# Performance work log

Measured on AMD Instinct MI355X. Metric: run time of the kernel, lower is better.

Reference implementation:

```python
import jax, jax.numpy as jnp
import numpy as np

B, S = 2, 2048          # packed prefill: 2 sequences of 2048 tokens
T = B * S
HID = 3584
H, KV, D = 16, 8, 256   # query heads, kv heads, head_dim (num_groups = 2)
SCALE = 256.0 ** -0.5   # query_pre_attn_scalar ** -0.5
SOFTCAP = 50.0
WINDOW = 1024           # sliding_window (window_size_left)
ROPE_THETA = 10000.0


def _rope_cos_sin():
    # TGI PositionRotaryEmbedding: per-token cos/sin of shape [T, D//2]
    inv_freq = 1.0 / (ROPE_THETA ** (np.arange(0, D, 2, dtype=np.float32) / D))
    pos = np.tile(np.arange(S, dtype=np.float32), B)  # positions restart per sequence
    freqs = pos[:, None] * inv_freq[None, :]          # [T, D/2]
    return jnp.asarray(np.cos(freqs)), jnp.asarray(np.sin(freqs))


def _apply_rope(x, cos, sin):
    # neox-style rotate-half; x: [T, h, D], cos/sin: [T, D/2]
    x1, x2 = x[..., : D // 2], x[..., D // 2 :]
    c, s = cos[:, None, :], sin[:, None, :]
    return jnp.concatenate([x1 * c - x2 * s, x2 * c + x1 * s], axis=-1)


def setup_inputs() -> dict:
    key = jax.random.key(0)
    k1, k2, k3 = jax.random.split(key, 3)
    cos, sin = _rope_cos_sin()
    return {
        "hidden_states": jax.random.normal(k1, (T, HID), dtype=jnp.float32),
        "cos": cos,
        "sin": sin,
        "w_qkv": jax.random.normal(k2, ((H + 2 * KV) * D, HID), dtype=jnp.float32) * 0.02,
        "w_o": jax.random.normal(k3, (HID, H * D), dtype=jnp.float32) * 0.02,
    }


def reference(hidden_states, cos, sin, w_qkv, w_o):
    qkv = hidden_states @ w_qkv.T                      # [T, (H+2KV)*D]
    q = qkv[:, : H * D].reshape(T, H, D)
    k = qkv[:, H * D : (H + KV) * D].reshape(T, KV, D)
    v = qkv[:, (H + KV) * D :].reshape(T, KV, D)

    q = _apply_rope(q, cos, sin)
    k = _apply_rope(k, cos, sin)

    # unpack varlen batch (equal-length sequences)
    q = q.reshape(B, S, H, D)
    # GQA: repeat each kv head num_groups=2 times (kv_head_mapping)
    k = jnp.repeat(k.reshape(B, S, KV, D), H // KV, axis=2)
    v = jnp.repeat(v.reshape(B, S, KV, D), H // KV, axis=2)

    scores = jnp.einsum("bqhd,bkhd->bhqk", q, k) * SCALE
    scores = SOFTCAP * jnp.tanh(scores / SOFTCAP)      # logit softcapping

    i = jnp.arange(S)[:, None]
    j = jnp.arange(S)[None, :]
    allowed = (j <= i) & (j >= i - WINDOW)             # causal + sliding window left
    scores = jnp.where(allowed[None, None], scores, jnp.finfo(scores.dtype).min)

    probs = jax.nn.softmax(scores, axis=-1)
    out = jnp.einsum("bhqk,bkhd->bqhd", probs, v)      # [B, S, H, D]
    return out.reshape(T, H * D) @ w_o.T               # [T, HID]
```

## Files before the change

kernel.cpp:

```cpp
#include <hip/hip_runtime.h>

typedef __bf16 bf16x8 __attribute__((ext_vector_type(8)));
typedef __bf16 bf16x4 __attribute__((ext_vector_type(4)));
typedef float  f32x4  __attribute__((ext_vector_type(4)));

#define AS1 __attribute__((address_space(1)))
#define AS3 __attribute__((address_space(3)))

__device__ __forceinline__ void async16(const void* g, void* l) {
  __builtin_amdgcn_global_load_lds((const AS1 void*)g, (AS3 void*)l, 16, 0, 0);
}

static constexpr int T_   = 4096;
static constexpr int Sq   = 2048;
static constexpr int HID  = 3584;
static constexpr int NH   = 16;
static constexpr int NKV  = 8;
static constexpr int DH   = 256;
static constexpr float SCALE_   = 0.0625f;
static constexpr float SOFTCAP_ = 50.0f;
static constexpr int WINDOW_    = 1024;

__global__ __launch_bounds__(256) void cast2_f32_bf16(const float4* __restrict__ a,
                                                      bf16x4* __restrict__ oa, int n4a,
                                                      const float4* __restrict__ b,
                                                      bf16x4* __restrict__ ob, int n4b) {
  int i = blockIdx.x * 256 + threadIdx.x;
  int stride = gridDim.x * 256;
  int ntot = n4a + n4b;
  for (; i < ntot; i += stride) {
    const float4 v = (i < n4a) ? a[i] : b[i - n4a];
    bf16x4 o;
    o[0] = (__bf16)v.x; o[1] = (__bf16)v.y; o[2] = (__bf16)v.z; o[3] = (__bf16)v.w;
    if (i < n4a) oa[i] = o; else ob[i - n4a] = o;
  }
}


#define VMW(N) do { asm volatile("s_waitcnt vmcnt(" #N ")" ::: "memory"); \
                    __builtin_amdgcn_sched_barrier(0); } while (0)

#define PHASE(SEL, CK, I0, KK, LOADB, STAGE)                                   \
  {                                                                            \
    bf16x8 a_[4];                                                              \
    _Pragma("unroll") for (int ii_ = 0; ii_ < 4; ++ii_)                        \
      a_[ii_] = *(const bf16x8*)&lA[SEL][aBase + (CK) + ((I0) + ii_) * 1024];  \
    if (LOADB) {                                                               \
      _Pragma("unroll") for (int j_ = 0; j_ < 4; ++j_)                         \
        bfr[j_][KK] = *(const bf16x8*)&lB[SEL][bBase + (CK) + j_ * 1024];      \
    }                                                                          \
    STAGE;                                                                     \
    __builtin_amdgcn_s_barrier();                                              \
    asm volatile("s_waitcnt lgkmcnt(0)" ::: "memory");                         \
    __builtin_amdgcn_sched_barrier(0);                                         \
    __builtin_amdgcn_s_setprio(1);                                             \
    _Pragma("unroll") for (int ii_ = 0; ii_ < 4; ++ii_)                        \
      _Pragma("unroll") for (int j_ = 0; j_ < 4; ++j_)                         \
        acc[(I0) + ii_][j_] = __builtin_amdgcn_mfma_f32_16x16x32_bf16(         \
            a_[ii_], bfr[j_][KK], acc[(I0) + ii_][j_], 0, 0, 0);               \
    __builtin_amdgcn_s_setprio(0);                                             \
    __builtin_amdgcn_sched_barrier(0);                                         \
    __builtin_amdgcn_s_barrier();                                              \
  }

template <bool OUT_BF16>
__global__ __launch_bounds__(512, 2) void gemm_bt8(const __bf16* __restrict__ A,
                                                   const __bf16* __restrict__ B,
                                                   __bf16* __restrict__ Cb,
                                                   float* __restrict__ Cf,
                                                   int M, int N, int K) {
  __shared__ __attribute__((aligned(16))) __bf16 lA[2][256 * 64];
  __shared__ __attribute__((aligned(16))) __bf16 lB[2][256 * 64];

  const int tid  = threadIdx.x;
  const int w    = tid >> 6;
  const int lane = tid & 63;
  const int wm   = w >> 2;
  const int wn   = w & 3;
  const int mrow = lane & 15;
  const int quad = lane >> 4;
  const int sw   = mrow & 7;

  const int gx = gridDim.x, gy = gridDim.y;
  const int orig = blockIdx.y * gx + blockIdx.x;
  int tileN, tileM;
  {
    int ccols, crows;
    if ((gx % 4) == 0 && (gy % 2) == 0)      { ccols = 4; crows = 2; }
    else if ((gx % 2) == 0 && (gy % 4) == 0) { ccols = 2; crows = 4; }
    else                                     { ccols = 1; crows = 1; }
    if (ccols * crows == 8) {
      const int cw = gx / ccols, ch = gy / crows;
      const int xcd = orig & 7, loc = orig >> 3;
      const int cx = xcd % ccols, cy = xcd / ccols;
      const int ln = loc % cw,    lm = loc / cw;
      tileN = (cx * cw + ln) * 256;
      tileM = (cy * ch + lm) * 256;
    } else {
      tileN = blockIdx.x * 256;
      tileM = blockIdx.y * 256;
    }
  }

  const int srow   = tid >> 3;
  const int schunk = (tid & 7) ^ (srow & 7);
  const int k64  = K << 6;
  const int k128 = K << 7;
  const __bf16* pa = A + (size_t)(tileM + srow) * K + schunk * 8;
  const __bf16* pb = B + (size_t)(tileN + srow) * K + schunk * 8;

  auto stage_half = [&](__bf16* lbase, int lrow, const __bf16* lanePtr, int koff) {
    async16(lanePtr + koff,       &lbase[(lrow + w * 8) * 64]);
    async16(lanePtr + koff + k64, &lbase[(lrow + 64 + w * 8) * 64]);
  };

  const int cK0 = (quad ^ sw) * 8;
  const int cK1 = cK0 ^ 32;
  const int aBase = (wm * 128 + mrow) * 64;
  const int bBase = (wn * 64 + mrow) * 64;

  f32x4 acc[8][4];
#pragma unroll
  for (int i = 0; i < 8; ++i)
#pragma unroll
    for (int j = 0; j < 4; ++j) acc[i][j] = (f32x4){0.f, 0.f, 0.f, 0.f};

  const int NT = K >> 6;
  const int NI = NT >> 1;

  stage_half(lB[0], 0,   pb, 0);
  stage_half(lB[0], 128, pb, k128);
  stage_half(lA[0], 0,   pa, 0);
  stage_half(lA[0], 128, pa, k128);
  stage_half(lB[1], 0,   pb, 64);
  stage_half(lB[1], 128, pb, 64 + k128);
  VMW(4);
  __builtin_amdgcn_s_barrier();

  for (int it = 0; it < NI; ++it) {
    const int t    = 2 * it;
    const bool more = (it + 1 < NI);
    const int kA1 = (t + 1) << 6;
    const int k2  = (t + 2) << 6;
    const int k3  = (t + 3) << 6;

    bf16x8 bfr[4][2];

    PHASE(0, cK0, 0, 0, true,
          { stage_half(lA[1], 0, pa, kA1); });
    PHASE(0, cK1, 0, 1, true,
          { stage_half(lA[1], 128, pa, kA1 + k128); });
    PHASE(0, cK0, 4, 0, false,
          { if (more) stage_half(lB[0], 0, pb, k2); });
    PHASE(0, cK1, 4, 1, false,
          { if (more) { stage_half(lB[0], 128, pb, k2 + k128); VMW(4); }
            else VMW(0); });
    PHASE(1, cK0, 0, 0, true,
          { if (more) stage_half(lA[0], 0, pa, k2); });
    PHASE(1, cK1, 0, 1, true,
          { if (more) stage_half(lA[0], 128, pa, k2 + k128); });
    PHASE(1, cK0, 4, 0, false,
          { if (more) stage_half(lB[1], 0, pb, k3); });
    PHASE(1, cK1, 4, 1, false,
          { if (more) { stage_half(lB[1], 128, pb, k3 + k128); VMW(4); }
            else VMW(0); });
  }

#pragma unroll
  for (int i = 0; i < 8; ++i) {
    const int row0 = tileM + wm * 128 + i * 16 + quad * 4;
#pragma unroll
    for (int j = 0; j < 4; ++j) {
      const int col = tileN + wn * 64 + j * 16 + mrow;
#pragma unroll
      for (int r = 0; r < 4; ++r) {
        if constexpr (OUT_BF16)
          Cb[(size_t)(row0 + r) * N + col] = (__bf16)acc[i][j][r];
        else
          Cf[(size_t)(row0 + r) * N + col] = acc[i][j][r];
      }
    }
  }
}

__global__ __launch_bounds__(256) void aux_fused(const __bf16* __restrict__ qkv,
                                                 const float* __restrict__ cosb,
                                                 const float* __restrict__ sinb,
                                                 __bf16* __restrict__ qout,
                                                 __bf16* __restrict__ kout,
                                                 __bf16* __restrict__ vt,
                                                 const float4* __restrict__ wo,
                                                 bf16x4* __restrict__ wo_bf) {
  __shared__ __bf16 tile[64][72];
  const int blk = blockIdx.x;
  const int tid = threadIdx.x;

  if (blk < 4096) {
    const int t = blk;
    const int b = t >> 11, s = t & (Sq - 1);
    const int d = tid & 127;
    const int half = tid >> 7;
    const float c  = cosb[t * 128 + d];
    const float sn = sinb[t * 128 + d];
    const size_t base = (size_t)t * 8192;
#pragma unroll
    for (int it = 0; it < 12; ++it) {
      int seg = it * 2 + half;
      float x1 = (float)qkv[base + seg * 256 + d];
      float x2 = (float)qkv[base + seg * 256 + 128 + d];
      float o1 = x1 * c - x2 * sn;
      float o2 = x2 * c + x1 * sn;
      if (seg < 16) {
        size_t o = ((size_t)(b * NH + seg) * Sq + s) * DH + d;
        qout[o] = (__bf16)o1;
        qout[o + 128] = (__bf16)o2;
      } else {
        int kvh = seg - 16;
        size_t o = ((size_t)(b * NKV + kvh) * Sq + s) * DH + d;
        kout[o] = (__bf16)o1;
        kout[o + 128] = (__bf16)o2;
      }
    }
  } else if (blk < 6144) {
    const int flat = blk - 4096;
    const int bx  = flat & 127;
    const int bkv = flat >> 7;
    const int b = bkv >> 3, kv = bkv & 7;
    const int st0 = (bx >> 2) * 64;
    const int dt0 = (bx & 3) * 64;
#pragma unroll
    for (int it = 0; it < 2; ++it) {
      int g = it * 256 + tid;
      int r = g >> 3, cc = (g & 7) * 8;
      const __bf16* src = qkv + (size_t)(b * Sq + st0 + r) * 8192 + 6144 + kv * 256 + dt0 + cc;
      bf16x8 v = *(const bf16x8*)src;
#pragma unroll
      for (int j = 0; j < 8; ++j) tile[r][cc + j] = v[j];
    }
    __syncthreads();
#pragma unroll
    for (int it = 0; it < 2; ++it) {
      int g = it * 256 + tid;
      int r = g >> 3, cc = (g & 7) * 8;
      bf16x8 v;
#pragma unroll
      for (int j = 0; j < 8; ++j) v[j] = tile[cc + j][r];
      *(bf16x8*)(vt + ((size_t)bkv * DH + dt0 + r) * Sq + st0 + cc) = v;
    }
  } else {
    const int n4 = HID * 4096 / 4;
    int i = (blk - 6144) * 256 + tid;
    const int stride = 1024 * 256;
    for (; i < n4; i += stride) {
      float4 v = wo[i];
      bf16x4 o;
      o[0] = (__bf16)v.x; o[1] = (__bf16)v.y; o[2] = (__bf16)v.z; o[3] = (__bf16)v.w;
      wo_bf[i] = o;
    }
  }
}

template <int MODE>
__device__ __forceinline__ void softcap_tile(const f32x4 sc[4], float lrun[4],
                                             __bf16* Pl, int pbase, int mrow,
                                             int kt, int qi) {
#pragma unroll
  for (int j = 0; j < 4; ++j) {
    const int kj = kt + j * 16 + mrow;
#pragma unroll
    for (int r = 0; r < 4; ++r) {
      float z = sc[j][r] * (SCALE_ / SOFTCAP_);
      float z2 = z * z;
      float u = __builtin_fmaf(z2, 0.13333333f, -0.33333333f);
      float th = z * __builtin_fmaf(z2, u, 1.0f);
      float pe = __builtin_fmaf(th, 72.134752f, -72.134752f);
      if (MODE == 1) pe = (kj <= qi + r) ? pe : -1000.0f;
      if (MODE == 2) pe = (kj >= qi + r - WINDOW_) ? pe : -1000.0f;
      float p = __builtin_amdgcn_exp2f(pe);
      lrun[r] += p;
      Pl[pbase + r * 72 + j * 16 + mrow] = (__bf16)p;
    }
  }
}

__global__ __launch_bounds__(256, 2) void attn_kernel(const __bf16* __restrict__ q,
                                                      const __bf16* __restrict__ k,
                                                      const __bf16* __restrict__ vt,
                                                      __bf16* __restrict__ out) {
  __shared__ __bf16 Kl[64 * 256];
  __shared__ __bf16 Vl[256 * 64];
  __shared__ __bf16 Pl[4 * 1152];

  const int bid0 = blockIdx.x;
  const int gidx = (bid0 & 7) * 128 + (bid0 >> 3);
  const int grp  = gidx >> 5;
  const int qt   = 31 - (gidx & 31);
  const int h    = grp & 15;
  const int b    = grp >> 4;
  const int kvh  = h >> 1;
  const int q0   = qt * 64;
  const int tid = threadIdx.x, w = tid >> 6, lane = tid & 63;
  const int mrow = lane & 15, quad = lane >> 4;
  const int sw = mrow & 7;

  bf16x8 qf[8];
  const __bf16* qbase = q + ((size_t)(b * NH + h) * Sq + q0 + w * 16 + mrow) * DH;
#pragma unroll
  for (int kf = 0; kf < 8; ++kf) qf[kf] = *(const bf16x8*)(qbase + kf * 32 + quad * 8);

  f32x4 o[16];
#pragma unroll
  for (int n = 0; n < 16; ++n) o[n] = (f32x4){0.f, 0.f, 0.f, 0.f};
  float lrun[4] = {0.f, 0.f, 0.f, 0.f};

  int kt_lo = q0 - WINDOW_; if (kt_lo < 0) kt_lo = 0;
  const __bf16* kbase = k + (size_t)(b * NKV + kvh) * Sq * DH;
  const __bf16* vbase = vt + (size_t)(b * NKV + kvh) * DH * Sq;
  const int qi = q0 + w * 16 + quad * 4;
  const int pbase = w * 1152 + quad * 4 * 72;

  for (int kt = kt_lo; kt <= q0; kt += 64) {
#pragma unroll
    for (int it = 0; it < 8; ++it) {
      int g = it * 256 + tid;
      int rk = g >> 5, uk = g & 31;
      const __bf16* gk = kbase + (size_t)(kt + rk) * DH + (uk ^ (rk & 7)) * 8;
      async16(gk, &Kl[(it * 256 + w * 64) * 8]);
    }
#pragma unroll
    for (int it = 0; it < 8; ++it) {
      int g = it * 256 + tid;
      int rv = g >> 3, uv = g & 7;
      const __bf16* gv = vbase + (size_t)rv * Sq + kt + (uv ^ (rv & 7)) * 8;
      async16(gv, &Vl[(it * 256 + w * 64) * 8]);
    }
    __syncthreads();

    f32x4 sc[4];
#pragma unroll
    for (int j = 0; j < 4; ++j) sc[j] = (f32x4){0.f, 0.f, 0.f, 0.f};
#pragma unroll
    for (int kf = 0; kf < 8; ++kf)
#pragma unroll
      for (int j = 0; j < 4; ++j) {
        bf16x8 kfr = *(const bf16x8*)&Kl[(j * 16 + mrow) * 256 + ((kf * 4 + quad) ^ sw) * 8];
        sc[j] = __builtin_amdgcn_mfma_f32_16x16x32_bf16(qf[kf], kfr, sc[j], 0, 0, 0);
      }

    if (kt == q0)                 softcap_tile<1>(sc, lrun, Pl, pbase, mrow, kt, qi);
    else if (kt == q0 - WINDOW_)  softcap_tile<2>(sc, lrun, Pl, pbase, mrow, kt, qi);
    else                          softcap_tile<0>(sc, lrun, Pl, pbase, mrow, kt, qi);

    bf16x8 pf0 = *(const bf16x8*)&Pl[w * 1152 + mrow * 72 + 0 * 32 + quad * 8];
    bf16x8 pf1 = *(const bf16x8*)&Pl[w * 1152 + mrow * 72 + 1 * 32 + quad * 8];

#pragma unroll
    for (int kk = 0; kk < 2; ++kk) {
      bf16x8 pf = kk ? pf1 : pf0;
#pragma unroll
      for (int n = 0; n < 16; ++n) {
        bf16x8 vf = *(const bf16x8*)&Vl[(n * 16 + mrow) * 64 + ((kk * 4 + quad) ^ sw) * 8];
        o[n] = __builtin_amdgcn_mfma_f32_16x16x32_bf16(pf, vf, o[n], 0, 0, 0);
      }
    }
    __syncthreads();
  }

#pragma unroll
  for (int m = 1; m < 16; m <<= 1)
#pragma unroll
    for (int r = 0; r < 4; ++r) lrun[r] += __shfl_xor(lrun[r], m, 64);

  float inv[4];
#pragma unroll
  for (int r = 0; r < 4; ++r) inv[r] = 1.f / lrun[r];
  const size_t trow = (size_t)(b * Sq + q0 + w * 16 + quad * 4);
#pragma unroll
  for (int n = 0; n < 16; ++n)
#pragma unroll
    for (int r = 0; r < 4; ++r)
      out[(trow + r) * 4096 + h * DH + n * 16 + mrow] = (__bf16)(o[n][r] * inv[r]);
}

extern "C" void kernel_launch(void* const* d_in, const int* in_sizes, int n_in,
                              void* d_out, int out_size, void* d_ws, size_t ws_size,
                              hipStream_t stream) {
  (void)in_sizes; (void)n_in; (void)out_size; (void)ws_size;
  const float* hs   = (const float*)d_in[0];
  const float* cosb = (const float*)d_in[1];
  const float* sinb = (const float*)d_in[2];
  const float* wqkv = (const float*)d_in[3];
  const float* wo   = (const float*)d_in[4];
  float* out = (float*)d_out;
  char* ws = (char*)d_ws;

  __bf16* hs_bf   = (__bf16*)(ws + 0);
  __bf16* wo_bf   = (__bf16*)(ws + 0);
  __bf16* wqkv_bf = (__bf16*)(ws + 29360128);
  __bf16* attn_bf = (__bf16*)(ws + 29360128);
  __bf16* qkv_bf  = (__bf16*)(ws + 88080384);
  __bf16* q_bf    = (__bf16*)(ws + 155189248);
  __bf16* k_bf    = (__bf16*)(ws + 188743680);
  __bf16* vt_bf   = (__bf16*)(ws + 205520896);

  cast2_f32_bf16<<<2048, 256, 0, stream>>>((const float4*)hs, (bf16x4*)hs_bf, T_ * HID / 4,
                                           (const float4*)wqkv, (bf16x4*)wqkv_bf, 8192 * HID / 4);

  gemm_bt8<true><<<dim3(8192 / 256, T_ / 256), 512, 0, stream>>>(
      hs_bf, wqkv_bf, qkv_bf, nullptr, T_, 8192, HID);

  aux_fused<<<7168, 256, 0, stream>>>(qkv_bf, cosb, sinb, q_bf, k_bf, vt_bf,
                                      (const float4*)wo, (bf16x4*)wo_bf);

  attn_kernel<<<dim3(2 * NH * (Sq / 64)), 256, 0, stream>>>(q_bf, k_bf, vt_bf, attn_bf);

  gemm_bt8<false><<<dim3(HID / 256, T_ / 256), 512, 0, stream>>>(
      attn_bf, wo_bf, nullptr, out, T_, HID, 4096);
}
```

Baseline: 701.9 us.

## Software-pipeline LDS fragment reads one phase ahead in bf16 GEMM main loop

Restructures the GEMM inner loop so LDS fragment reads for the next phase go into a second register set (aX/aY ping-pong) while the current phase's MFMAs run. This replaces the old two barriers plus lgkmcnt(0) wait per phase with one barrier per phase. Global-to-LDS staging is interleaved as before, with the vmcnt wait thresholds adjusted. It aims to hide LDS read latency behind MFMA work, at the cost of more registers and more subtle ordering between the async LDS writes and the reads.

After: 709.6 us. No clear change (+1.1%).

```diff
diff --git a/kernel.cpp b/kernel.cpp
--- a/kernel.cpp
+++ b/kernel.cpp
@@ -40,28 +40,25 @@
 #define VMW(N) do { asm volatile("s_waitcnt vmcnt(" #N ")" ::: "memory"); \
                     __builtin_amdgcn_sched_barrier(0); } while (0)
 
-#define PHASE(SEL, CK, I0, KK, LOADB, STAGE)                                   \
-  {                                                                            \
-    bf16x8 a_[4];                                                              \
-    _Pragma("unroll") for (int ii_ = 0; ii_ < 4; ++ii_)                        \
-      a_[ii_] = *(const bf16x8*)&lA[SEL][aBase + (CK) + ((I0) + ii_) * 1024];  \
-    if (LOADB) {                                                               \
-      _Pragma("unroll") for (int j_ = 0; j_ < 4; ++j_)                         \
-        bfr[j_][KK] = *(const bf16x8*)&lB[SEL][bBase + (CK) + j_ * 1024];      \
-    }                                                                          \
-    STAGE;                                                                     \
-    __builtin_amdgcn_s_barrier();                                              \
-    asm volatile("s_waitcnt lgkmcnt(0)" ::: "memory");                         \
-    __builtin_amdgcn_sched_barrier(0);                                         \
-    __builtin_amdgcn_s_setprio(1);                                             \
-    _Pragma("unroll") for (int ii_ = 0; ii_ < 4; ++ii_)                        \
-      _Pragma("unroll") for (int j_ = 0; j_ < 4; ++j_)                         \
-        acc[(I0) + ii_][j_] = __builtin_amdgcn_mfma_f32_16x16x32_bf16(         \
-            a_[ii_], bfr[j_][KK], acc[(I0) + ii_][j_], 0, 0, 0);               \
-    __builtin_amdgcn_s_setprio(0);                                             \
-    __builtin_amdgcn_sched_barrier(0);                                         \
-    __builtin_amdgcn_s_barrier();                                              \
-  }
+#define BAR() do { asm volatile("" ::: "memory"); \
+                   __builtin_amdgcn_s_barrier();  \
+                   asm volatile("" ::: "memory"); } while (0)
+
+#define RD_A(dst, SEL, CK, I0)                                                 \
+  _Pragma("unroll") for (int ii_ = 0; ii_ < 4; ++ii_)                          \
+    dst[ii_] = *(const bf16x8*)&lA[SEL][aBase + (CK) + ((I0) + ii_) * 1024];
+
+#define RD_B(KK, SEL, CK)                                                      \
+  _Pragma("unroll") for (int j_ = 0; j_ < 4; ++j_)                             \
+    bfr[j_][KK] = *(const bf16x8*)&lB[SEL][bBase + (CK) + j_ * 1024];
+
+#define MFMA4(aSet, KK, I0)                                                    \
+  __builtin_amdgcn_s_setprio(1);                                               \
+  _Pragma("unroll") for (int ii_ = 0; ii_ < 4; ++ii_)                          \
+    _Pragma("unroll") for (int j_ = 0; j_ < 4; ++j_)                           \
+      acc[(I0) + ii_][j_] = __builtin_amdgcn_mfma_f32_16x16x32_bf16(           \
+          aSet[ii_], bfr[j_][KK], acc[(I0) + ii_][j_], 0, 0, 0);               \
+  __builtin_amdgcn_s_setprio(0);
 
 template <bool OUT_BF16>
 __global__ __launch_bounds__(512, 2) void gemm_bt8(const __bf16* __restrict__ A,
@@ -135,7 +132,10 @@
   stage_half(lB[1], 0,   pb, 64);
   stage_half(lB[1], 128, pb, 64 + k128);
   VMW(4);
-  __builtin_amdgcn_s_barrier();
+  BAR();
+
+  bf16x8 aX[4], aY[4], bfr[4][2];
+  RD_A(aX, 0, cK0, 0); RD_B(0, 0, cK0);
 
   for (int it = 0; it < NI; ++it) {
     const int t    = 2 * it;
@@ -144,26 +144,40 @@
     const int k2  = (t + 2) << 6;
     const int k3  = (t + 3) << 6;
 
-    bf16x8 bfr[4][2];
-
-    PHASE(0, cK0, 0, 0, true,
-          { stage_half(lA[1], 0, pa, kA1); });
-    PHASE(0, cK1, 0, 1, true,
-          { stage_half(lA[1], 128, pa, kA1 + k128); });
-    PHASE(0, cK0, 4, 0, false,
-          { if (more) stage_half(lB[0], 0, pb, k2); });
-    PHASE(0, cK1, 4, 1, false,
-          { if (more) { stage_half(lB[0], 128, pb, k2 + k128); VMW(4); }
-            else VMW(0); });
-    PHASE(1, cK0, 0, 0, true,
-          { if (more) stage_half(lA[0], 0, pa, k2); });
-    PHASE(1, cK1, 0, 1, true,
-          { if (more) stage_half(lA[0], 128, pa, k2 + k128); });
-    PHASE(1, cK0, 4, 0, false,
-          { if (more) stage_half(lB[1], 0, pb, k3); });
-    PHASE(1, cK1, 4, 1, false,
-          { if (more) { stage_half(lB[1], 128, pb, k3 + k128); VMW(4); }
-            else VMW(0); });
+    RD_A(aY, 0, cK1, 0); RD_B(1, 0, cK1);
+    stage_half(lA[1], 0, pa, kA1);
+    MFMA4(aX, 0, 0);
+    BAR();
+    RD_A(aX, 0, cK0, 4);
+    stage_half(lA[1], 128, pa, kA1 + k128);
+    MFMA4(aY, 1, 0);
+    BAR();
+    RD_A(aY, 0, cK1, 4);
+    if (more) stage_half(lB[0], 0, pb, k2);
+    MFMA4(aX, 0, 4);
+    if (more) VMW(2); else VMW(0);
+    BAR();
+    RD_A(aX, 1, cK0, 0); RD_B(0, 1, cK0);
+    if (more) stage_half(lB[0], 128, pb, k2 + k128);
+    MFMA4(aY, 1, 4);
+    BAR();
+    RD_A(aY, 1, cK1, 0); RD_B(1, 1, cK1);
+    if (more) stage_half(lA[0], 0, pa, k2);
+    MFMA4(aX, 0, 0);
+    BAR();
+    RD_A(aX, 1, cK0, 4);
+    if (more) stage_half(lA[0], 128, pa, k2 + k128);
+    MFMA4(aY, 1, 0);
+    BAR();
+    RD_A(aY, 1, cK1, 4);
+    if (more) stage_half(lB[1], 0, pb, k3);
+    MFMA4(aX, 0, 4);
+    if (more) VMW(2); else VMW(0);
+    BAR();
+    RD_A(aX, 0, cK0, 0); RD_B(0, 0, cK0);
+    if (more) stage_half(lB[1], 128, pb, k3 + k128);
+    MFMA4(aY, 1, 4);
+    BAR();
   }
 
 #pragma unroll
```
